# Kernel optimization log

Hardware: AMD Instinct MI355X
Metric: run time of the kernel (lower is better)

The kernel has to match this reference:

```python
import jax, jax.numpy as jnp
import numpy as np

N, E = 50000, 800000          # nodes, edges (avg degree 16)
D_IN, D_H, D_OUT = 128, 128, 64
BN_EPS = 1e-5


def setup_inputs() -> dict:
    key = jax.random.key(0)
    ks = jax.random.split(key, 8)
    g = lambda k, shp, s: jax.random.normal(k, shp, jnp.float32) * s
    return {
        "x": jax.random.normal(ks[0], (N, D_IN), jnp.float32),
        "edge_index": jax.random.randint(ks[1], (2, E), 0, N),
        # SAGEConv layer 1: lin_l (neighbors, with bias), lin_r (root, no bias)
        "Wl1": g(ks[2], (D_IN, D_H), 0.05),
        "Wr1": g(ks[3], (D_IN, D_H), 0.05),
        "b1": jnp.zeros((D_H,), jnp.float32),
        # BatchNorm1d(hidden)
        "gamma": jnp.ones((D_H,), jnp.float32),
        "beta": jnp.zeros((D_H,), jnp.float32),
        # SAGEConv layer 2
        "Wl2": g(ks[4], (D_H, D_OUT), 0.05),
        "Wr2": g(ks[5], (D_H, D_OUT), 0.05),
        "b2": jnp.zeros((D_OUT,), jnp.float32),
    }


def _sage_conv(x, src, dst, Wl, Wr, b):
    """PyG SAGEConv (mean aggr): lin_l(mean_{j in N(i)} x_j) + lin_r(x_i)."""
    n = x.shape[0]
    agg = jax.ops.segment_sum(x[src], dst, num_segments=n)            # [N, d]
    cnt = jax.ops.segment_sum(jnp.ones((src.shape[0],), x.dtype), dst,
                              num_segments=n)                          # [N]
    agg = agg / jnp.maximum(cnt, 1.0)[:, None]                         # mean, 0 for isolated
    return agg @ Wl + x @ Wr + b


def _batch_norm(x, gamma, beta):
    """Training-mode BatchNorm1d: batch stats over the node axis, biased var."""
    mu = jnp.mean(x, axis=0)
    var = jnp.var(x, axis=0)
    return gamma * (x - mu) * jax.lax.rsqrt(var + BN_EPS) + beta


def reference(x, edge_index, Wl1, Wr1, b1, gamma, beta, Wl2, Wr2, b2):
    src, dst = edge_index[0], edge_index[1]
    h = _sage_conv(x, src, dst, Wl1, Wr1, b1)
    h = jax.nn.relu(_batch_norm(h, gamma, beta))
    # dropout is identity in eval / deterministic reference
    return _sage_conv(h, src, dst, Wl2, Wr2, b2)
```

## Files before the change

kernel.cpp:

```cpp
#include <hip/hip_runtime.h>
#include <hip/hip_bf16.h>
#include <hip/hip_fp8.h>

#define DIN   128
#define DH    128
#define DOUTC 64
#define BN_EPS 1e-5f

typedef __attribute__((ext_vector_type(8))) short bf16x8;
typedef __attribute__((ext_vector_type(4))) float f32x4;
typedef __attribute__((ext_vector_type(2))) float f32x2;

#ifndef __has_builtin
#define __has_builtin(x) 0
#endif
#if __has_builtin(__builtin_amdgcn_cvt_pk_f32_fp8) && __has_builtin(__builtin_amdgcn_cvt_pk_fp8_f32)
#define HW_FP8 1
#else
#define HW_FP8 0
#endif

__device__ inline unsigned short f2bf(float f) {
    __hip_bfloat16 b = __float2bfloat16(f);
    return *reinterpret_cast<unsigned short*>(&b);
}
__device__ inline float bf2f(unsigned short u) {
    return __uint_as_float(((unsigned int)u) << 16);
}
__device__ inline void fp8x4_to_f32(unsigned int w, float* o) {
#if HW_FP8
    f32x2 lo = __builtin_amdgcn_cvt_pk_f32_fp8((int)w, false);
    f32x2 hi = __builtin_amdgcn_cvt_pk_f32_fp8((int)w, true);
    o[0] = lo.x; o[1] = lo.y; o[2] = hi.x; o[3] = hi.y;
#else
    #pragma unroll
    for (int c = 0; c < 4; ++c) {
        __hip_fp8_e4m3 q; q.__x = (__hip_fp8_storage_t)((w >> (8 * c)) & 0xFF);
        o[c] = (float)q;
    }
#endif
}
__device__ inline unsigned int f32x4_to_fp8(float a, float b, float c, float d) {
#if HW_FP8
    int p = __builtin_amdgcn_cvt_pk_fp8_f32(a, b, 0, false);
    p = __builtin_amdgcn_cvt_pk_fp8_f32(c, d, p, true);
    return (unsigned int)p;
#else
    __hip_fp8_e4m3 qa(a), qb(b), qc(c), qd(d);
    return (unsigned int)qa.__x | ((unsigned int)qb.__x << 8) |
           ((unsigned int)qc.__x << 16) | ((unsigned int)qd.__x << 24);
#endif
}

__device__ inline void block_excl_scan_256(const int* __restrict__ arr,
                                           int* __restrict__ excl,
                                           int* __restrict__ wsum, int tid)
{
    int lane = tid & 63, w = tid >> 6;
    int v = arr[tid];
    int inc = v;
    #pragma unroll
    for (int off = 1; off < 64; off <<= 1) {
        int t = __shfl_up(inc, off, 64);
        if (lane >= off) inc += t;
    }
    if (lane == 63) wsum[w] = inc;
    __syncthreads();
    if (tid == 0) {
        int s = 0;
        #pragma unroll
        for (int i = 0; i < 4; ++i) { int t = wsum[i]; wsum[i] = s; s += t; }
    }
    __syncthreads();
    excl[tid] = inc - v + wsum[w];
    __syncthreads();
}

__global__ __launch_bounds__(256) void prep_kernel(
    const float* __restrict__ x, unsigned char* __restrict__ xq,
    const float* __restrict__ Wl1, const float* __restrict__ Wr1,
    const float* __restrict__ Wl2, const float* __restrict__ Wr2,
    unsigned short* __restrict__ W1p, unsigned short* __restrict__ W2p,
    const int* __restrict__ ei, int* __restrict__ cursor,
    unsigned int* __restrict__ coarse,
    int total8, int cvtB, int E, int nb, int cap)
{
    __shared__ int hist[256], lstart[256], gbase[256], wsum[4];
    __shared__ unsigned int staged[4096];
    const int b = blockIdx.x;
    const int tid = threadIdx.x;

    if (b < cvtB) {
        int i = b * 256 + tid;
        if (i >= total8) return;
        float4 a = ((const float4*)x)[2 * i];
        float4 c = ((const float4*)x)[2 * i + 1];
        uint2 pk;
        pk.x = f32x4_to_fp8(a.x, a.y, a.z, a.w);
        pk.y = f32x4_to_fp8(c.x, c.y, c.z, c.w);
        *(uint2*)(xq + (size_t)i * 8) = pk;
        return;
    }
    if (b < cvtB + 192) {
        int region = (b - cvtB) >> 6;
        int idx = ((b - cvtB) & 63) * 256 + tid;
        int k = idx >> 7, c = idx & 127;
        int d = ((k >> 5) * 8 + (c >> 4)) * 512 + ((k >> 3) & 3) * 128 + (c & 15) * 8 + (k & 7);
        if (region == 0)      W1p[d] = f2bf(Wl1[idx]);
        else if (region == 1) W1p[128 * 128 + d] = f2bf(Wr1[idx]);
        else {
            float v = (c < 64) ? Wl2[k * 64 + c] : Wr2[k * 64 + (c - 64)];
            W2p[d] = f2bf(v);
        }
        return;
    }

    const int chunkBase = (b - cvtB - 192) * 4096;
    hist[tid] = 0;
    __syncthreads();

    unsigned int rec[16]; int pos[16]; int bb[16];
    #pragma unroll
    for (int i = 0; i < 16; ++i) {
        int e = chunkBase + i * 256 + tid;
        if (e < E) {
            int s = ei[e], d = ei[E + e];
            rec[i] = ((unsigned int)d << 16) | (unsigned int)s;
            bb[i]  = d >> 8;
            pos[i] = atomicAdd(&hist[bb[i]], 1);
        } else bb[i] = -1;
    }
    __syncthreads();

    block_excl_scan_256(hist, lstart, wsum, tid);

    if (tid < nb) {
        int c = hist[tid];
        gbase[tid] = c ? atomicAdd(&cursor[tid], c) : 0;
    }
    __syncthreads();

    #pragma unroll
    for (int i = 0; i < 16; ++i)
        if (bb[i] >= 0) staged[lstart[bb[i]] + pos[i]] = rec[i];
    __syncthreads();

    int total = min(4096, E - chunkBase);
    for (int i = tid; i < total; i += 256) {
        unsigned int r = staged[i];
        int bk  = (int)(r >> 24);
        int gp  = gbase[bk] + (i - lstart[bk]);
        if (gp < cap) coarse[(size_t)bk * cap + gp] = r;
    }
}

__global__ __launch_bounds__(256) void bin_fine(
    const int* __restrict__ cursor, const unsigned int* __restrict__ coarse,
    unsigned short* __restrict__ sorted, int* __restrict__ deg,
    int* __restrict__ row_start, int n, int cap)
{
    __shared__ int hist[256], pstart[256], cur2[256], wsum[4];
    const int b = blockIdx.x, tid = threadIdx.x;
    const int cnt = min(cursor[b], cap);
    const unsigned int* src = coarse + (size_t)b * cap;

    hist[tid] = 0;
    __syncthreads();

    int nIter = (cnt + 255) >> 8;
    for (int i = 0; i < nIter; ++i) {
        int idx = i * 256 + tid;
        if (idx < cnt) atomicAdd(&hist[(src[idx] >> 16) & 255], 1);
    }
    __syncthreads();

    block_excl_scan_256(hist, pstart, wsum, tid);
    cur2[tid] = pstart[tid];
    __syncthreads();

    for (int i = 0; i < nIter; ++i) {
        int idx = i * 256 + tid;
        if (idx < cnt) {
            unsigned int r = src[idx];
            int dl = (r >> 16) & 255;
            int p  = atomicAdd(&cur2[dl], 1);
            sorted[(size_t)b * cap + p] = (unsigned short)(r & 0xFFFFu);
        }
    }

    int node = b * 256 + tid;
    if (node < n) {
        deg[node]       = hist[tid];
        row_start[node] = b * cap + pstart[tid];
    }
}

__global__ __launch_bounds__(256) void gemm1_fused(
    const unsigned char* __restrict__ xq, const float* __restrict__ x,
    const int* __restrict__ row_start, const int* __restrict__ deg,
    const unsigned short* __restrict__ sorted,
    const unsigned short* __restrict__ W1p, const float* __restrict__ bias,
    unsigned short* __restrict__ hb,
    float* __restrict__ bn_sum, float* __restrict__ bn_sumsq, int n)
{
    __shared__ unsigned short G[64][136];
    __shared__ float red[2][4][128];

    const int block_row = blockIdx.x * 64;
    const int tid  = threadIdx.x;
    const int wave = tid >> 6;
    const int lane = tid & 63;
    const int q    = lane >> 4;
    const int m16  = lane & 15;

    {
        int sub = lane & 7, oct = lane >> 3;
        #pragma unroll
        for (int grp = 0; grp < 2; ++grp) {
            int lr = wave * 16 + grp * 8 + oct;
            int g  = block_row + lr;
            float acc[16];
            #pragma unroll
            for (int j = 0; j < 16; ++j) acc[j] = 0.f;
            int d = 0;
            if (g < n) {
                int base = row_start[g];
                d = deg[g];
                int t = 0;
                for (; t + 8 <= d; t += 8) {
                    uint4 raws[8];
                    #pragma unroll
                    for (int u = 0; u < 8; ++u) {
                        int s = (int)sorted[base + t + u];
                        raws[u] = ((const uint4*)(xq + (size_t)s * DIN))[sub];
                    }
                    #pragma unroll
                    for (int u = 0; u < 8; ++u) {
                        const unsigned int* w = (const unsigned int*)&raws[u];
                        #pragma unroll
                        for (int c = 0; c < 4; ++c) {
                            float o4[4];
                            fp8x4_to_f32(w[c], o4);
                            acc[c*4+0] += o4[0]; acc[c*4+1] += o4[1];
                            acc[c*4+2] += o4[2]; acc[c*4+3] += o4[3];
                        }
                    }
                }
                for (; t < d; ++t) {
                    int s = (int)sorted[base + t];
                    uint4 raw = ((const uint4*)(xq + (size_t)s * DIN))[sub];
                    const unsigned int* w = (const unsigned int*)&raw;
                    #pragma unroll
                    for (int c = 0; c < 4; ++c) {
                        float o4[4];
                        fp8x4_to_f32(w[c], o4);
                        acc[c*4+0] += o4[0]; acc[c*4+1] += o4[1];
                        acc[c*4+2] += o4[2]; acc[c*4+3] += o4[3];
                    }
                }
            }
            float inv = 1.0f / fmaxf((float)d, 1.0f);
            unsigned short t16[16];
            #pragma unroll
            for (int j = 0; j < 16; ++j) t16[j] = f2bf(acc[j] * inv);
            *(uint4*)&G[lr][sub * 16]     = ((uint4*)t16)[0];
            *(uint4*)&G[lr][sub * 16 + 8] = ((uint4*)t16)[1];
        }
    }

    f32x4 acc[8];
    #pragma unroll
    for (int nt = 0; nt < 8; ++nt) acc[nt] = (f32x4){0.f, 0.f, 0.f, 0.f};

    const int grow = block_row + wave * 16 + m16;
    #pragma unroll
    for (int ks = 0; ks < 4; ++ks) {
        bf16x8 ag = *(const bf16x8*)&G[wave * 16 + m16][ks * 32 + q * 8];
        const unsigned short* wp0 = W1p + (size_t)ks * 8 * 512;
        #pragma unroll
        for (int nt = 0; nt < 8; ++nt) {
            bf16x8 b = *(const bf16x8*)(wp0 + nt * 512 + lane * 8);
            acc[nt] = __builtin_amdgcn_mfma_f32_16x16x32_bf16(ag, b, acc[nt], 0, 0, 0);
        }
        bf16x8 ax;
        {
            float4 f0 = {0.f,0.f,0.f,0.f}, f1 = {0.f,0.f,0.f,0.f};
            if (grow < n) {
                const float* xr = x + (size_t)grow * DIN + ks * 32 + q * 8;
                f0 = *(const float4*)xr;
                f1 = *(const float4*)(xr + 4);
            }
            unsigned short t[8];
            t[0]=f2bf(f0.x); t[1]=f2bf(f0.y); t[2]=f2bf(f0.z); t[3]=f2bf(f0.w);
            t[4]=f2bf(f1.x); t[5]=f2bf(f1.y); t[6]=f2bf(f1.z); t[7]=f2bf(f1.w);
            ax = *(bf16x8*)t;
        }
        const unsigned short* wp1 = W1p + (size_t)(4 + ks) * 8 * 512;
        #pragma unroll
        for (int nt = 0; nt < 8; ++nt) {
            bf16x8 b = *(const bf16x8*)(wp1 + nt * 512 + lane * 8);
            acc[nt] = __builtin_amdgcn_mfma_f32_16x16x32_bf16(ax, b, acc[nt], 0, 0, 0);
        }
    }

    float psum[8], psq[8];
    #pragma unroll
    for (int nt = 0; nt < 8; ++nt) {
        int col = nt * 16 + m16;
        float bv = bias[col];
        float s = 0.f, ssq = 0.f;
        #pragma unroll
        for (int reg = 0; reg < 4; ++reg) {
            int g = block_row + wave * 16 + q * 4 + reg;
            float v = acc[nt][reg] + bv;
            if (g < n) {
                hb[(size_t)g * DH + col] = f2bf(v);
                s += v; ssq += v * v;
            }
        }
        psum[nt] = s; psq[nt] = ssq;
    }
    #pragma unroll
    for (int nt = 0; nt < 8; ++nt) {
        psum[nt] += __shfl_xor(psum[nt], 16, 64);
        psum[nt] += __shfl_xor(psum[nt], 32, 64);
        psq[nt]  += __shfl_xor(psq[nt], 16, 64);
        psq[nt]  += __shfl_xor(psq[nt], 32, 64);
    }
    if (lane < 16) {
        #pragma unroll
        for (int nt = 0; nt < 8; ++nt) {
            red[0][wave][nt * 16 + lane] = psum[nt];
            red[1][wave][nt * 16 + lane] = psq[nt];
        }
    }
    __syncthreads();
    if (tid < 128) {
        float s = red[0][0][tid] + red[0][1][tid] + red[0][2][tid] + red[0][3][tid];
        float ssq = red[1][0][tid] + red[1][1][tid] + red[1][2][tid] + red[1][3][tid];
        atomicAdd(&bn_sum[tid], s);
        atomicAdd(&bn_sumsq[tid], ssq);
    }
}

__global__ __launch_bounds__(256) void gemm2p_mfma(
    const unsigned short* __restrict__ hb,
    const float* __restrict__ bn_sum, const float* __restrict__ bn_sumsq,
    const float* __restrict__ gamma, const float* __restrict__ beta,
    const unsigned short* __restrict__ W2p, const float* __restrict__ bias,
    unsigned short* __restrict__ P, float* __restrict__ out, int n)
{
    __shared__ float s_scale[128], s_shift[128];

    const int block_row = blockIdx.x * 64;
    const int tid  = threadIdx.x;
    const int wave = tid >> 6;
    const int lane = tid & 63;
    const int q    = lane >> 4;
    const int m16  = lane & 15;

    if (tid < 128) {
        float invN = 1.0f / (float)n;
        float mu  = bn_sum[tid] * invN;
        float var = bn_sumsq[tid] * invN - mu * mu;
        float sc  = gamma[tid] * rsqrtf(var + BN_EPS);
        s_scale[tid] = sc;
        s_shift[tid] = beta[tid] - mu * sc;
    }
    __syncthreads();

    f32x4 acc[8];
    #pragma unroll
    for (int nt = 0; nt < 8; ++nt) acc[nt] = (f32x4){0.f, 0.f, 0.f, 0.f};

    const int grow = block_row + wave * 16 + m16;
    #pragma unroll
    for (int ks = 0; ks < 4; ++ks) {
        bf16x8 a;
        {
            int kbase = ks * 32 + q * 8;
            float4 sc0 = *(const float4*)&s_scale[kbase];
            float4 sc1 = *(const float4*)&s_scale[kbase + 4];
            float4 sh0 = *(const float4*)&s_shift[kbase];
            float4 sh1 = *(const float4*)&s_shift[kbase + 4];
            unsigned short t[8] = {0,0,0,0,0,0,0,0};
            if (grow < n) {
                uint4 raw = *(const uint4*)(hb + (size_t)grow * DH + kbase);
                const unsigned short* u = (const unsigned short*)&raw;
                t[0] = f2bf(fmaxf(bf2f(u[0]) * sc0.x + sh0.x, 0.f));
                t[1] = f2bf(fmaxf(bf2f(u[1]) * sc0.y + sh0.y, 0.f));
                t[2] = f2bf(fmaxf(bf2f(u[2]) * sc0.z + sh0.z, 0.f));
                t[3] = f2bf(fmaxf(bf2f(u[3]) * sc0.w + sh0.w, 0.f));
                t[4] = f2bf(fmaxf(bf2f(u[4]) * sc1.x + sh1.x, 0.f));
                t[5] = f2bf(fmaxf(bf2f(u[5]) * sc1.y + sh1.y, 0.f));
                t[6] = f2bf(fmaxf(bf2f(u[6]) * sc1.z + sh1.z, 0.f));
                t[7] = f2bf(fmaxf(bf2f(u[7]) * sc1.w + sh1.w, 0.f));
            }
            a = *(bf16x8*)t;
        }
        const unsigned short* wp = W2p + (size_t)ks * 8 * 512;
        #pragma unroll
        for (int nt = 0; nt < 8; ++nt) {
            bf16x8 b = *(const bf16x8*)(wp + nt * 512 + lane * 8);
            acc[nt] = __builtin_amdgcn_mfma_f32_16x16x32_bf16(a, b, acc[nt], 0, 0, 0);
        }
    }

    #pragma unroll
    for (int nt = 0; nt < 4; ++nt) {
        int col = nt * 16 + m16;
        #pragma unroll
        for (int reg = 0; reg < 4; ++reg) {
            int g = block_row + wave * 16 + q * 4 + reg;
            if (g < n) P[(size_t)g * DOUTC + col] = f2bf(acc[nt][reg]);
        }
    }
    #pragma unroll
    for (int nt = 4; nt < 8; ++nt) {
        int col = (nt - 4) * 16 + m16;
        float bv = bias[col];
        #pragma unroll
        for (int reg = 0; reg < 4; ++reg) {
            int g = block_row + wave * 16 + q * 4 + reg;
            if (g < n) out[(size_t)g * DOUTC + col] = acc[nt][reg] + bv;
        }
    }
}

__global__ __launch_bounds__(256) void agg_gather64_add(
    const int* __restrict__ row_start, const int* __restrict__ deg,
    const unsigned short* __restrict__ sorted, const unsigned short* __restrict__ P,
    float* __restrict__ out, int n)
{
    int wid  = (blockIdx.x * 256 + threadIdx.x) >> 6;
    int lane = threadIdx.x & 63;
    int sub = lane & 7, oct = lane >> 3;
    int r = wid * 8 + oct;
    if (r >= n) return;

    float acc[8];
    #pragma unroll
    for (int j = 0; j < 8; ++j) acc[j] = 0.f;

    int base = row_start[r];
    int d    = deg[r];
    int t = 0;
    for (; t + 8 <= d; t += 8) {
        uint4 raws[8];
        #pragma unroll
        for (int u = 0; u < 8; ++u) {
            int s = (int)sorted[base + t + u];
            raws[u] = ((const uint4*)(P + (size_t)s * DOUTC))[sub];
        }
        #pragma unroll
        for (int u = 0; u < 8; ++u) {
            const unsigned short* us = (const unsigned short*)&raws[u];
            #pragma unroll
            for (int j = 0; j < 8; ++j) acc[j] += bf2f(us[j]);
        }
    }
    for (; t < d; ++t) {
        int s = (int)sorted[base + t];
        uint4 raw = ((const uint4*)(P + (size_t)s * DOUTC))[sub];
        const unsigned short* us = (const unsigned short*)&raw;
        #pragma unroll
        for (int j = 0; j < 8; ++j) acc[j] += bf2f(us[j]);
    }
    float inv = 1.0f / fmaxf((float)d, 1.0f);
    float* op = out + (size_t)r * DOUTC + sub * 8;
    float4 c0 = *(float4*)op;
    float4 c1 = *((float4*)op + 1);
    c0.x += acc[0] * inv; c0.y += acc[1] * inv;
    c0.z += acc[2] * inv; c0.w += acc[3] * inv;
    c1.x += acc[4] * inv; c1.y += acc[5] * inv;
    c1.z += acc[6] * inv; c1.w += acc[7] * inv;
    *(float4*)op = c0;
    *((float4*)op + 1) = c1;
}

extern "C" void kernel_launch(void* const* d_in, const int* in_sizes, int n_in,
                              void* d_out, int out_size, void* d_ws, size_t ws_size,
                              hipStream_t stream)
{
    const float* x     = (const float*)d_in[0];
    const int*   ei    = (const int*)  d_in[1];
    const float* Wl1   = (const float*)d_in[2];
    const float* Wr1   = (const float*)d_in[3];
    const float* b1    = (const float*)d_in[4];
    const float* gamma = (const float*)d_in[5];
    const float* beta  = (const float*)d_in[6];
    const float* Wl2   = (const float*)d_in[7];
    const float* Wr2   = (const float*)d_in[8];
    const float* b2    = (const float*)d_in[9];
    float*       out   = (float*)d_out;

    const int N = in_sizes[0] / DIN;
    const int E = in_sizes[1] / 2;

    const int NB  = (N + 255) >> 8;
    int cap = (E / NB) * 3 / 2 + 256;
    cap = (cap + 255) & ~255;

    float* bn_sum   = (float*)d_ws;
    float* bn_sumsq = bn_sum + DH;
    int* cursor     = (int*)(bn_sumsq + DH);
    int* deg        = cursor + 256;
    int* row_start  = deg + N;
    unsigned int* coarse   = (unsigned int*)(row_start + N);
    unsigned short* sorted = (unsigned short*)(coarse + (size_t)NB * cap);
    unsigned short* hb     = sorted + (size_t)NB * cap;
    unsigned short* P      = hb + (size_t)N * DH;
    unsigned short* W1p    = P + (size_t)N * DOUTC;
    unsigned short* W2p    = W1p + 256 * 128;
    unsigned char*  xq     = (unsigned char*)(W2p + 128 * 128);

    hipMemsetAsync(bn_sum, 0, (2 * DH + 256) * sizeof(float), stream);

    dim3 blk(256);
    const int cvtB        = (N * DIN / 8 + 255) / 256;
    const int binA_blocks = (E + 4095) / 4096;
    const int gemm_blocks = (N + 63) / 64;
    const int g64_blocks  = ((N + 7) / 8 + 3) / 4;

    prep_kernel<<<cvtB + 192 + binA_blocks, blk, 0, stream>>>(
        x, xq, Wl1, Wr1, Wl2, Wr2, W1p, W2p,
        ei, cursor, coarse, N * DIN / 8, cvtB, E, NB, cap);

    bin_fine<<<NB, blk, 0, stream>>>(cursor, coarse, sorted, deg, row_start, N, cap);

    gemm1_fused<<<gemm_blocks, blk, 0, stream>>>(xq, x, row_start, deg, sorted,
                                                 W1p, b1, hb, bn_sum, bn_sumsq, N);

    gemm2p_mfma<<<gemm_blocks, blk, 0, stream>>>(hb, bn_sum, bn_sumsq,
                                                 gamma, beta, W2p, b2, P, out, N);

    agg_gather64_add<<<g64_blocks, blk, 0, stream>>>(row_start, deg, sorted,
                                                     P, out, N);
}
```

Measured before the change: 209.1 us.

## Double gemm1 block to 512 threads, one gather row per thread

Launches the fused aggregation+GEMM1 kernel with 512 threads per 64-row tile. Each group of 8 threads now gathers one node's neighbours instead of each thread handling two rows sequentially. The MFMA phase is split across 8 waves as 4 row blocks × 2 column halves. A block barrier is added before the MFMA phase because waves now read rows of the shared tile gathered by other waves. The aim is more memory-level parallelism in the irregular gather and lower per-thread register use. The cost is the extra barrier and duplicate loads of the root features x across column waves.

```diff
diff --git a/kernel.cpp b/kernel.cpp
--- a/kernel.cpp
+++ b/kernel.cpp
@@ -195,7 +195,7 @@
     }
 }
 
-__global__ __launch_bounds__(256) void gemm1_fused(
+__global__ __launch_bounds__(512) void gemm1_fused(
     const unsigned char* __restrict__ xq, const float* __restrict__ x,
     const int* __restrict__ row_start, const int* __restrict__ deg,
     const unsigned short* __restrict__ sorted,
@@ -208,48 +208,29 @@
 
     const int block_row = blockIdx.x * 64;
     const int tid  = threadIdx.x;
-    const int wave = tid >> 6;
-    const int lane = tid & 63;
-    const int q    = lane >> 4;
-    const int m16  = lane & 15;
 
     {
-        int sub = lane & 7, oct = lane >> 3;
-        #pragma unroll
-        for (int grp = 0; grp < 2; ++grp) {
-            int lr = wave * 16 + grp * 8 + oct;
-            int g  = block_row + lr;
-            float acc[16];
-            #pragma unroll
-            for (int j = 0; j < 16; ++j) acc[j] = 0.f;
-            int d = 0;
-            if (g < n) {
-                int base = row_start[g];
-                d = deg[g];
-                int t = 0;
-                for (; t + 8 <= d; t += 8) {
-                    uint4 raws[8];
-                    #pragma unroll
-                    for (int u = 0; u < 8; ++u) {
-                        int s = (int)sorted[base + t + u];
-                        raws[u] = ((const uint4*)(xq + (size_t)s * DIN))[sub];
-                    }
-                    #pragma unroll
-                    for (int u = 0; u < 8; ++u) {
-                        const unsigned int* w = (const unsigned int*)&raws[u];
-                        #pragma unroll
-                        for (int c = 0; c < 4; ++c) {
-                            float o4[4];
-                            fp8x4_to_f32(w[c], o4);
-                            acc[c*4+0] += o4[0]; acc[c*4+1] += o4[1];
-                            acc[c*4+2] += o4[2]; acc[c*4+3] += o4[3];
-                        }
-                    }
+        int group = tid >> 3;
+        int sub   = tid & 7;
+        int g = block_row + group;
+        float acc[16];
+        #pragma unroll
+        for (int j = 0; j < 16; ++j) acc[j] = 0.f;
+        int d = 0;
+        if (g < n) {
+            int base = row_start[g];
+            d = deg[g];
+            int t = 0;
+            for (; t + 8 <= d; t += 8) {
+                uint4 raws[8];
+                #pragma unroll
+                for (int u = 0; u < 8; ++u) {
+                    int s = (int)sorted[base + t + u];
+                    raws[u] = ((const uint4*)(xq + (size_t)s * DIN))[sub];
                 }
-                for (; t < d; ++t) {
-                    int s = (int)sorted[base + t];
-                    uint4 raw = ((const uint4*)(xq + (size_t)s * DIN))[sub];
-                    const unsigned int* w = (const unsigned int*)&raw;
+                #pragma unroll
+                for (int u = 0; u < 8; ++u) {
+                    const unsigned int* w = (const unsigned int*)&raws[u];
                     #pragma unroll
                     for (int c = 0; c < 4; ++c) {
                         float o4[4];
@@ -259,26 +240,46 @@
                     }
                 }
             }
-            float inv = 1.0f / fmaxf((float)d, 1.0f);
-            unsigned short t16[16];
-            #pragma unroll
-            for (int j = 0; j < 16; ++j) t16[j] = f2bf(acc[j] * inv);
-            *(uint4*)&G[lr][sub * 16]     = ((uint4*)t16)[0];
-            *(uint4*)&G[lr][sub * 16 + 8] = ((uint4*)t16)[1];
-        }
-    }
-
-    f32x4 acc[8];
-    #pragma unroll
-    for (int nt = 0; nt < 8; ++nt) acc[nt] = (f32x4){0.f, 0.f, 0.f, 0.f};
-
-    const int grow = block_row + wave * 16 + m16;
+            for (; t < d; ++t) {
+                int s = (int)sorted[base + t];
+                uint4 raw = ((const uint4*)(xq + (size_t)s * DIN))[sub];
+                const unsigned int* w = (const unsigned int*)&raw;
+                #pragma unroll
+                for (int c = 0; c < 4; ++c) {
+                    float o4[4];
+                    fp8x4_to_f32(w[c], o4);
+                    acc[c*4+0] += o4[0]; acc[c*4+1] += o4[1];
+                    acc[c*4+2] += o4[2]; acc[c*4+3] += o4[3];
+                }
+            }
+        }
+        float inv = 1.0f / fmaxf((float)d, 1.0f);
+        unsigned short t16[16];
+        #pragma unroll
+        for (int j = 0; j < 16; ++j) t16[j] = f2bf(acc[j] * inv);
+        *(uint4*)&G[group][sub * 16]     = ((uint4*)t16)[0];
+        *(uint4*)&G[group][sub * 16 + 8] = ((uint4*)t16)[1];
+    }
+    __syncthreads();
+
+    const int wave   = tid >> 6;
+    const int lane   = tid & 63;
+    const int rowblk = wave & 3;
+    const int colblk = wave >> 2;
+    const int q      = lane >> 4;
+    const int m16    = lane & 15;
+
+    f32x4 acc[4];
+    #pragma unroll
+    for (int nt = 0; nt < 4; ++nt) acc[nt] = (f32x4){0.f, 0.f, 0.f, 0.f};
+
+    const int grow = block_row + rowblk * 16 + m16;
     #pragma unroll
     for (int ks = 0; ks < 4; ++ks) {
-        bf16x8 ag = *(const bf16x8*)&G[wave * 16 + m16][ks * 32 + q * 8];
-        const unsigned short* wp0 = W1p + (size_t)ks * 8 * 512;
-        #pragma unroll
-        for (int nt = 0; nt < 8; ++nt) {
+        bf16x8 ag = *(const bf16x8*)&G[rowblk * 16 + m16][ks * 32 + q * 8];
+        const unsigned short* wp0 = W1p + (size_t)ks * 8 * 512 + colblk * 4 * 512;
+        #pragma unroll
+        for (int nt = 0; nt < 4; ++nt) {
             bf16x8 b = *(const bf16x8*)(wp0 + nt * 512 + lane * 8);
             acc[nt] = __builtin_amdgcn_mfma_f32_16x16x32_bf16(ag, b, acc[nt], 0, 0, 0);
         }
@@ -295,23 +296,23 @@
             t[4]=f2bf(f1.x); t[5]=f2bf(f1.y); t[6]=f2bf(f1.z); t[7]=f2bf(f1.w);
             ax = *(bf16x8*)t;
         }
-        const unsigned short* wp1 = W1p + (size_t)(4 + ks) * 8 * 512;
-        #pragma unroll
-        for (int nt = 0; nt < 8; ++nt) {
+        const unsigned short* wp1 = W1p + (size_t)(4 + ks) * 8 * 512 + colblk * 4 * 512;
+        #pragma unroll
+        for (int nt = 0; nt < 4; ++nt) {
             bf16x8 b = *(const bf16x8*)(wp1 + nt * 512 + lane * 8);
             acc[nt] = __builtin_amdgcn_mfma_f32_16x16x32_bf16(ax, b, acc[nt], 0, 0, 0);
         }
     }
 
-    float psum[8], psq[8];
-    #pragma unroll
-    for (int nt = 0; nt < 8; ++nt) {
-        int col = nt * 16 + m16;
+    float psum[4], psq[4];
+    #pragma unroll
+    for (int nt = 0; nt < 4; ++nt) {
+        int col = colblk * 64 + nt * 16 + m16;
         float bv = bias[col];
         float s = 0.f, ssq = 0.f;
         #pragma unroll
         for (int reg = 0; reg < 4; ++reg) {
-            int g = block_row + wave * 16 + q * 4 + reg;
+            int g = block_row + rowblk * 16 + q * 4 + reg;
             float v = acc[nt][reg] + bv;
             if (g < n) {
                 hb[(size_t)g * DH + col] = f2bf(v);
@@ -321,7 +322,7 @@
         psum[nt] = s; psq[nt] = ssq;
     }
     #pragma unroll
-    for (int nt = 0; nt < 8; ++nt) {
+    for (int nt = 0; nt < 4; ++nt) {
         psum[nt] += __shfl_xor(psum[nt], 16, 64);
         psum[nt] += __shfl_xor(psum[nt], 32, 64);
         psq[nt]  += __shfl_xor(psq[nt], 16, 64);
@@ -329,9 +330,10 @@
     }
     if (lane < 16) {
         #pragma unroll
-        for (int nt = 0; nt < 8; ++nt) {
-            red[0][wave][nt * 16 + lane] = psum[nt];
-            red[1][wave][nt * 16 + lane] = psq[nt];
+        for (int nt = 0; nt < 4; ++nt) {
+            int col = colblk * 64 + nt * 16 + lane;
+            red[0][rowblk][col] = psum[nt];
+            red[1][rowblk][col] = psq[nt];
         }
     }
     __syncthreads();
@@ -528,8 +530,8 @@
 
     bin_fine<<<NB, blk, 0, stream>>>(cursor, coarse, sorted, deg, row_start, N, cap);
 
-    gemm1_fused<<<gemm_blocks, blk, 0, stream>>>(xq, x, row_start, deg, sorted,
-                                                 W1p, b1, hb, bn_sum, bn_sumsq, N);
+    gemm1_fused<<<gemm_blocks, dim3(512), 0, stream>>>(xq, x, row_start, deg, sorted,
+                                                       W1p, b1, hb, bn_sum, bn_sumsq, N);
 
     gemm2p_mfma<<<gemm_blocks, blk, 0, stream>>>(hb, bn_sum, bn_sumsq,
                                                  gamma, beta, W2p, b2, P, out, N);
```

Result: slower. 217.3 us (+4.0%).
